# Kernel optimization log

Hardware: AMD Instinct MI355X
Metric: run time of the kernel (lower is better)

The kernel has to match this reference:

```python
import jax, jax.numpy as jnp
import numpy as np

N = 50000
E = 800000
IN_C = 128
HID = 128
OUT_C = 2


def _linear_params(key, fan_in, fan_out):
    k1, k2 = jax.random.split(key)
    bound = 1.0 / np.sqrt(fan_in)
    W = jax.random.uniform(k1, (fan_in, fan_out), jnp.float32, -bound, bound)
    b = jax.random.uniform(k2, (fan_out,), jnp.float32, -bound, bound)
    return W, b


def setup_inputs() -> dict:
    key = jax.random.key(0)
    ks = jax.random.split(key, 9)
    x = jax.random.normal(ks[0], (N, IN_C), jnp.float32)
    edge_index = jax.random.randint(ks[1], (2, E), 0, N, jnp.int64)
    W1a, b1a = _linear_params(ks[2], IN_C, HID)
    W1b, b1b = _linear_params(ks[3], HID, HID)
    W2a, b2a = _linear_params(ks[4], HID, HID)
    W2b, b2b = _linear_params(ks[5], HID, HID)
    Wfc, bfc = _linear_params(ks[6], HID, OUT_C)
    return {
        "x": x, "edge_index": edge_index,
        "W1a": W1a, "b1a": b1a, "W1b": W1b, "b1b": b1b,
        "W2a": W2a, "b2a": b2a, "W2b": W2b, "b2b": b2b,
        "Wfc": Wfc, "bfc": bfc,
    }


def _gin_conv(x, src, dst, Wa, ba, Wb, bb):
    # GINConv with eps=0: h = MLP(x + sum_{j in N(i)} x_j)
    agg = jax.ops.segment_sum(x[src], dst, num_segments=N)  # [N, d]
    h = x + agg
    h = jax.nn.relu(h @ Wa + ba)
    return h @ Wb + bb


def reference(x, edge_index, W1a, b1a, W1b, b1b, W2a, b2a, W2b, b2b, Wfc, bfc):
    src, dst = edge_index[0], edge_index[1]  # messages flow src -> dst
    h = _gin_conv(x, src, dst, W1a, b1a, W1b, b1b)
    h = jax.nn.relu(h)
    # dropout is identity in eval mode
    h = _gin_conv(h, src, dst, W2a, b2a, W2b, b2b)
    return h @ Wfc + bfc  # [N, 2]
```

## Files before the change

### kernel.cpp

```cpp
#include <hip/hip_runtime.h>

#define N_NODES 50000
#define N_EDGES 800000
#define NBUK    196
#define B_A     1024
#define EPB     782
#define CAPB    5120

typedef unsigned short u16;
typedef unsigned int   u32;
typedef __bf16 bf16x8 __attribute__((ext_vector_type(8)));
typedef float  f32x4  __attribute__((ext_vector_type(4)));

__device__ __forceinline__ float bf_lo(u32 v){ return __uint_as_float(v << 16); }
__device__ __forceinline__ float bf_hi(u32 v){ return __uint_as_float(v & 0xffff0000u); }
__device__ __forceinline__ u32 bf_pack(float a, float b){
    u32 ua = __float_as_uint(a), ub = __float_as_uint(b);
    ua += 0x7fffu + ((ua >> 16) & 1u);
    ub += 0x7fffu + ((ub >> 16) & 1u);
    return (ua >> 16) | (ub & 0xffff0000u);
}
__device__ __forceinline__ u16 f2bf(float a){
    u32 ua = __float_as_uint(a);
    ua += 0x7fffu + ((ua >> 16) & 1u);
    return (u16)(ua >> 16);
}
__device__ __forceinline__ void addu4(uint4 v, float* a){
    a[0] += bf_lo(v.x); a[1] += bf_hi(v.x);
    a[2] += bf_lo(v.y); a[3] += bf_hi(v.y);
    a[4] += bf_lo(v.z); a[5] += bf_hi(v.z);
    a[6] += bf_lo(v.w); a[7] += bf_hi(v.w);
}

__device__ __forceinline__ int blockScan256(int v, int* ws, int t) {
    int lane = t & 63, w = t >> 6;
    #pragma unroll
    for (int off = 1; off < 64; off <<= 1) {
        int u = __shfl_up(v, off);
        if (lane >= off) v += u;
    }
    if (lane == 63) ws[w] = v;
    __syncthreads();
    int add = 0;
    for (int k = 0; k < w; k++) add += ws[k];
    return v + add;
}

__launch_bounds__(256)
__global__ void binA_kernel(const int* __restrict__ esrc, const int* __restrict__ edst,
                            u32* __restrict__ binned, int* __restrict__ startTab,
                            int* __restrict__ cntTab,
                            const float* __restrict__ xsrc, u32* __restrict__ xb,
                            const float* __restrict__ W1a, const float* __restrict__ W1b,
                            const float* __restrict__ W2a, const float* __restrict__ W2b,
                            const float* __restrict__ Wfc, const float* __restrict__ b2b,
                            const float* __restrict__ bfc,
                            u16* __restrict__ wt1a, u16* __restrict__ wt1b,
                            u16* __restrict__ wt2a,
                            float* __restrict__ Wc, float* __restrict__ bc) {
    int t = threadIdx.x, blk = blockIdx.x;
    if (blk >= B_A) {
        int b = blk - B_A;
        if (b < 192) {
            int g  = b * 256 + t;
            int mi = g >> 14;
            int p  = g & 16383;
            int k  = p >> 7, m = p & 127;
            const float* src = (mi == 0) ? W1a : (mi == 1) ? W1b : W2a;
            u16* dst         = (mi == 0) ? wt1a : (mi == 1) ? wt1b : wt2a;
            dst[m * 128 + k] = f2bf(src[k * 128 + m]);
        } else {
            int j = t >> 1, o = t & 1;
            float s = 0.f;
            for (int k = 0; k < 128; k++)
                s += W2b[j * 128 + k] * Wfc[k * 2 + o];
            Wc[j * 2 + o] = s;
            if (t < 2) {
                float s2 = 0.f;
                for (int k = 0; k < 128; k++)
                    s2 += b2b[k] * Wfc[k * 2 + t];
                bc[t] = s2 + bfc[t];
            }
        }
        return;
    }
    __shared__ int hist[NBUK];
    __shared__ int cur[NBUK];
    __shared__ u32 ebuf[EPB];
    __shared__ int ws[4];
    int base = blk * EPB;
    for (int i = t; i < NBUK; i += 256) hist[i] = 0;
    __syncthreads();
    for (int i = t; i < EPB; i += 256) {
        int gi = base + i;
        if (gi < N_EDGES) atomicAdd(&hist[edst[gi] >> 8], 1);
    }
    __syncthreads();
    int v = (t < NBUK) ? hist[t] : 0;
    int incl = blockScan256(v, ws, t);
    int excl = incl - v;
    if (t < NBUK) {
        startTab[t * B_A + blk] = excl;
        cntTab[t * B_A + blk]   = v;
        cur[t] = excl;
    }
    __syncthreads();
    for (int i = t; i < EPB; i += 256) {
        int gi = base + i;
        if (gi < N_EDGES) {
            int d = edst[gi], s = esrc[gi];
            int p = atomicAdd(&cur[d >> 8], 1);
            ebuf[p] = (u32)s | ((u32)(d & 255) << 16);
        }
    }
    __syncthreads();
    for (int i = t; i < EPB; i += 256)
        binned[base + i] = ebuf[i];
    const int total = N_NODES * 64;
    for (int i = blk * 256 + t; i < total; i += B_A * 256) {
        float2 f = ((const float2*)xsrc)[i];
        xb[i] = bf_pack(f.x, f.y);
    }
}

__launch_bounds__(256)
__global__ void binB_kernel(const u32* __restrict__ binned, const int* __restrict__ startTab,
                            const int* __restrict__ cntTab,
                            int2* __restrict__ span, int* __restrict__ csr) {
    __shared__ u32 ebuf[CAPB];
    __shared__ int cbuf[CAPB];
    __shared__ int runoff[B_A + 1];
    __shared__ int runstart[B_A];
    __shared__ int hist[256];
    __shared__ int cursor[256];
    __shared__ int ws[4];
    int b = blockIdx.x, t = threadIdx.x;
    int c4[4], s = 0;
    #pragma unroll
    for (int q = 0; q < 4; q++) {
        c4[q] = cntTab[b * B_A + t * 4 + q];
        s += c4[q];
    }
    int incl = blockScan256(s, ws, t);
    int rb = incl - s;
    #pragma unroll
    for (int q = 0; q < 4; q++) {
        int run = t * 4 + q;
        runoff[run]   = rb;
        runstart[run] = run * EPB + startTab[b * B_A + run];
        rb += c4[q];
    }
    if (t == 255) runoff[B_A] = incl;
    hist[t] = 0;
    __syncthreads();
    int tot = runoff[B_A];
    if (tot > CAPB) tot = CAPB;
    for (int i = t; i < tot; i += 256) {
        int lo = 0, hi = B_A;
        while (hi - lo > 1) {
            int mid = (lo + hi) >> 1;
            if (runoff[mid] <= i) lo = mid; else hi = mid;
        }
        ebuf[i] = binned[runstart[lo] + (i - runoff[lo])];
    }
    __syncthreads();
    for (int i = t; i < tot; i += 256)
        atomicAdd(&hist[ebuf[i] >> 16], 1);
    __syncthreads();
    int hv = hist[t];
    int hincl = blockScan256(hv, ws, t);
    int hexcl = hincl - hv;
    cursor[t] = hexcl;
    int gb = b * CAPB;
    int node = (b << 8) + t;
    if (node < N_NODES) span[node] = make_int2(gb + hexcl, gb + hexcl + hv);
    __syncthreads();
    for (int i = t; i < tot; i += 256) {
        u32 e = ebuf[i];
        int p = atomicAdd(&cursor[e >> 16], 1);
        cbuf[p] = (int)(e & 0xFFFFu);
    }
    __syncthreads();
    for (int i = t; i < tot; i += 256)
        csr[gb + i] = cbuf[i];
}

template<int MODE>
__launch_bounds__(256, 4)
__global__ void fconv_kernel(const u32* __restrict__ xb,
                             const u16* __restrict__ WA, const float* __restrict__ bA,
                             const u16* __restrict__ WB, const float* __restrict__ bB,
                             const float* __restrict__ Wc, const float* __restrict__ bc,
                             const int2* __restrict__ span, const int* __restrict__ csr,
                             u16* __restrict__ C, float2* __restrict__ out, int n) {
    __shared__ u16 As[64][136];
    int t = threadIdx.x;
    int row0 = blockIdx.x * 64;
    int w = t >> 6, lane = t & 63;
    int g4 = lane >> 4, l16 = lane & 15;
    const uint4* xp = (const uint4*)xb;
    #pragma unroll
    for (int p = 0; p < 4; p++) {
        int rl = w * 16 + p * 4 + g4;
        int node = row0 + rl;
        float a[8] = {0.f,0.f,0.f,0.f,0.f,0.f,0.f,0.f};
        if (node < n) {
            addu4(xp[(size_t)node * 16 + l16], a);
            int2 sp = span[node];
            int j = sp.x, jend = sp.y;
            for (; j + 8 <= jend; j += 8) {
                int s0 = csr[j],     s1 = csr[j + 1], s2 = csr[j + 2], s3 = csr[j + 3];
                int s4 = csr[j + 4], s5 = csr[j + 5], s6 = csr[j + 6], s7 = csr[j + 7];
                uint4 v0 = xp[(size_t)s0 * 16 + l16], v1 = xp[(size_t)s1 * 16 + l16];
                uint4 v2 = xp[(size_t)s2 * 16 + l16], v3 = xp[(size_t)s3 * 16 + l16];
                uint4 v4 = xp[(size_t)s4 * 16 + l16], v5 = xp[(size_t)s5 * 16 + l16];
                uint4 v6 = xp[(size_t)s6 * 16 + l16], v7 = xp[(size_t)s7 * 16 + l16];
                addu4(v0, a); addu4(v1, a); addu4(v2, a); addu4(v3, a);
                addu4(v4, a); addu4(v5, a); addu4(v6, a); addu4(v7, a);
            }
            for (; j + 4 <= jend; j += 4) {
                int s0 = csr[j], s1 = csr[j + 1], s2 = csr[j + 2], s3 = csr[j + 3];
                uint4 v0 = xp[(size_t)s0 * 16 + l16], v1 = xp[(size_t)s1 * 16 + l16];
                uint4 v2 = xp[(size_t)s2 * 16 + l16], v3 = xp[(size_t)s3 * 16 + l16];
                addu4(v0, a); addu4(v1, a); addu4(v2, a); addu4(v3, a);
            }
            for (; j < jend; j++)
                addu4(xp[(size_t)csr[j] * 16 + l16], a);
        }
        uint4 pk = make_uint4(bf_pack(a[0], a[1]), bf_pack(a[2], a[3]),
                              bf_pack(a[4], a[5]), bf_pack(a[6], a[7]));
        *(uint4*)&As[rl][l16 * 8] = pk;
    }

    int lm = l16, lq = g4;
    f32x4 acc[8];
    #pragma unroll
    for (int c = 0; c < 8; c++) acc[c] = (f32x4){0.f, 0.f, 0.f, 0.f};
    #pragma unroll
    for (int kk = 0; kk < 4; kk++) {
        bf16x8 af = *(const bf16x8*)&As[w * 16 + lm][kk * 32 + lq * 8];
        #pragma unroll
        for (int c = 0; c < 8; c++) {
            bf16x8 bf = *(const bf16x8*)(WA + (size_t)(c * 16 + lm) * 128 + kk * 32 + lq * 8);
            acc[c] = __builtin_amdgcn_mfma_f32_16x16x32_bf16(af, bf, acc[c], 0, 0, 0);
        }
    }
    if (MODE == 0) {
        #pragma unroll
        for (int c = 0; c < 8; c++) {
            int col = c * 16 + lm;
            float bcol = bA[col];
            #pragma unroll
            for (int r = 0; r < 4; r++) {
                float v = acc[c][r] + bcol;
                v = v > 0.f ? v : 0.f;
                As[w * 16 + lq * 4 + r][col] = f2bf(v);
            }
        }
        f32x4 acc2[8];
        #pragma unroll
        for (int c = 0; c < 8; c++) acc2[c] = (f32x4){0.f, 0.f, 0.f, 0.f};
        #pragma unroll
        for (int kk = 0; kk < 4; kk++) {
            bf16x8 af = *(const bf16x8*)&As[w * 16 + lm][kk * 32 + lq * 8];
            #pragma unroll
            for (int c = 0; c < 8; c++) {
                bf16x8 bf = *(const bf16x8*)(WB + (size_t)(c * 16 + lm) * 128 + kk * 32 + lq * 8);
                acc2[c] = __builtin_amdgcn_mfma_f32_16x16x32_bf16(af, bf, acc2[c], 0, 0, 0);
            }
        }
        #pragma unroll
        for (int c = 0; c < 8; c++) {
            int col = c * 16 + lm;
            float bcol = bB[col];
            #pragma unroll
            for (int r = 0; r < 4; r++) {
                int row = row0 + w * 16 + lq * 4 + r;
                if (row < n) {
                    float v = acc2[c][r] + bcol;
                    v = v > 0.f ? v : 0.f;
                    C[(size_t)row * 128 + col] = f2bf(v);
                }
            }
        }
    } else {
        float p0[4] = {0,0,0,0}, p1[4] = {0,0,0,0};
        #pragma unroll
        for (int c = 0; c < 8; c++) {
            int col = c * 16 + lm;
            float bcol = bA[col];
            float2 wc = ((const float2*)Wc)[col];
            #pragma unroll
            for (int r = 0; r < 4; r++) {
                float v = acc[c][r] + bcol;
                v = v > 0.f ? v : 0.f;
                p0[r] += v * wc.x;
                p1[r] += v * wc.y;
            }
        }
        #pragma unroll
        for (int off = 1; off < 16; off <<= 1) {
            #pragma unroll
            for (int r = 0; r < 4; r++) {
                p0[r] += __shfl_xor(p0[r], off);
                p1[r] += __shfl_xor(p1[r], off);
            }
        }
        if (lm == 0) {
            float b0 = bc[0], b1 = bc[1];
            #pragma unroll
            for (int r = 0; r < 4; r++) {
                int row = row0 + w * 16 + lq * 4 + r;
                if (row < n) out[row] = make_float2(p0[r] + b0, p1[r] + b1);
            }
        }
    }
}

extern "C" void kernel_launch(void* const* d_in, const int* in_sizes, int n_in,
                              void* d_out, int out_size, void* d_ws, size_t ws_size,
                              hipStream_t stream) {
    const float* x   = (const float*)d_in[0];
    const int*   ei  = (const int*)d_in[1];
    const float* W1a = (const float*)d_in[2];
    const float* b1a = (const float*)d_in[3];
    const float* W1b = (const float*)d_in[4];
    const float* b1b = (const float*)d_in[5];
    const float* W2a = (const float*)d_in[6];
    const float* b2a = (const float*)d_in[7];
    const float* W2b = (const float*)d_in[8];
    const float* b2b = (const float*)d_in[9];
    const float* Wfc = (const float*)d_in[10];
    const float* bfc = (const float*)d_in[11];

    const int* esrc = ei;
    const int* edst = ei + N_EDGES;

    char* w = (char*)d_ws;
    size_t off = 0;
    auto alloc = [&](size_t bytes) -> char* {
        char* p = w + off;
        off = (off + bytes + 255) & ~(size_t)255;
        return p;
    };
    int2*  span       = (int2*)alloc((size_t)N_NODES * 8);
    int*   startTab   = (int*)alloc((size_t)NBUK * B_A * 4);
    int*   cntTab     = (int*)alloc((size_t)NBUK * B_A * 4);
    int*   csr        = (int*)alloc((size_t)NBUK * CAPB * 4);
    u16*   wt1a       = (u16*)alloc(128 * 128 * 2);
    u16*   wt1b       = (u16*)alloc(128 * 128 * 2);
    u16*   wt2a       = (u16*)alloc(128 * 128 * 2);
    float* Wc         = (float*)alloc(256 * 4);
    float* bc         = (float*)alloc(2 * 4);
    u16*   bufA       = (u16*)alloc((size_t)N_NODES * 128 * 2);
    u16*   bufB       = (u16*)alloc((size_t)N_NODES * 128 * 2);
    u32*   binned     = (u32*)bufA;

    binA_kernel<<<B_A + 193, 256, 0, stream>>>(esrc, edst, binned, startTab, cntTab,
                                               x, (u32*)bufB,
                                               W1a, W1b, W2a, W2b, Wfc, b2b, bfc,
                                               wt1a, wt1b, wt2a, Wc, bc);
    binB_kernel<<<NBUK, 256, 0, stream>>>(binned, startTab, cntTab, span, csr);

    const int TILES = (N_NODES + 63) / 64;
    fconv_kernel<0><<<TILES, 256, 0, stream>>>((const u32*)bufB, wt1a, b1a, wt1b, b1b,
                                               nullptr, nullptr, span, csr,
                                               bufA, nullptr, N_NODES);
    fconv_kernel<1><<<TILES, 256, 0, stream>>>((const u32*)bufA, wt2a, b2a, nullptr, nullptr,
                                               Wc, bc, span, csr,
                                               nullptr, (float2*)d_out, N_NODES);
}
```

Before: 227.9 us.

## Halve bucket width to 128 nodes and gather runs per-thread in binB

The destination buckets shrink from 256 to 128 nodes, doubling the bucket count to 392 so binB launches twice as many smaller blocks with half the shared capacity. binB also drops the per-element binary search over run offsets and has each thread copy its own four runs sequentially. The goal is more parallelism and less shared memory per block in the binning stage. Sequential per-thread copies give uncoalesced, unbalanced loads, and the smaller CAPB raises the risk of bucket overflow truncating edges.

```diff
diff --git a/kernel.cpp b/kernel.cpp
--- a/kernel.cpp
+++ b/kernel.cpp
@@ -2,10 +2,10 @@
 
 #define N_NODES 50000
 #define N_EDGES 800000
-#define NBUK    196
+#define NBUK    392
 #define B_A     1024
 #define EPB     782
-#define CAPB    5120
+#define CAPB    2560
 
 typedef unsigned short u16;
 typedef unsigned int   u32;
@@ -93,24 +93,29 @@
     __syncthreads();
     for (int i = t; i < EPB; i += 256) {
         int gi = base + i;
-        if (gi < N_EDGES) atomicAdd(&hist[edst[gi] >> 8], 1);
-    }
-    __syncthreads();
-    int v = (t < NBUK) ? hist[t] : 0;
-    int incl = blockScan256(v, ws, t);
-    int excl = incl - v;
-    if (t < NBUK) {
-        startTab[t * B_A + blk] = excl;
-        cntTab[t * B_A + blk]   = v;
-        cur[t] = excl;
+        if (gi < N_EDGES) atomicAdd(&hist[edst[gi] >> 7], 1);
+    }
+    __syncthreads();
+    int c0 = 0, c1 = 0;
+    if (t < 196) { c0 = hist[2 * t]; c1 = hist[2 * t + 1]; }
+    int s2 = c0 + c1;
+    int incl = blockScan256(s2, ws, t);
+    int excl = incl - s2;
+    if (t < 196) {
+        startTab[(2 * t) * B_A + blk]     = excl;
+        cntTab[(2 * t) * B_A + blk]       = c0;
+        cur[2 * t] = excl;
+        startTab[(2 * t + 1) * B_A + blk] = excl + c0;
+        cntTab[(2 * t + 1) * B_A + blk]   = c1;
+        cur[2 * t + 1] = excl + c0;
     }
     __syncthreads();
     for (int i = t; i < EPB; i += 256) {
         int gi = base + i;
         if (gi < N_EDGES) {
             int d = edst[gi], s = esrc[gi];
-            int p = atomicAdd(&cur[d >> 8], 1);
-            ebuf[p] = (u32)s | ((u32)(d & 255) << 16);
+            int p = atomicAdd(&cur[d >> 7], 1);
+            ebuf[p] = (u32)s | ((u32)(d & 127) << 16);
         }
     }
     __syncthreads();
@@ -129,51 +134,48 @@
                             int2* __restrict__ span, int* __restrict__ csr) {
     __shared__ u32 ebuf[CAPB];
     __shared__ int cbuf[CAPB];
-    __shared__ int runoff[B_A + 1];
-    __shared__ int runstart[B_A];
-    __shared__ int hist[256];
-    __shared__ int cursor[256];
+    __shared__ int hist[128];
+    __shared__ int cursor[128];
     __shared__ int ws[4];
+    __shared__ int totsh;
     int b = blockIdx.x, t = threadIdx.x;
-    int c4[4], s = 0;
+    int c4[4], rs4[4], s = 0;
     #pragma unroll
     for (int q = 0; q < 4; q++) {
-        c4[q] = cntTab[b * B_A + t * 4 + q];
+        int run = t * 4 + q;
+        c4[q]  = cntTab[b * B_A + run];
+        rs4[q] = run * EPB + startTab[b * B_A + run];
         s += c4[q];
     }
     int incl = blockScan256(s, ws, t);
     int rb = incl - s;
+    if (t == 255) totsh = incl;
+    if (t < 128) hist[t] = 0;
+    __syncthreads();
     #pragma unroll
     for (int q = 0; q < 4; q++) {
-        int run = t * 4 + q;
-        runoff[run]   = rb;
-        runstart[run] = run * EPB + startTab[b * B_A + run];
-        rb += c4[q];
-    }
-    if (t == 255) runoff[B_A] = incl;
-    hist[t] = 0;
-    __syncthreads();
-    int tot = runoff[B_A];
+        int c = c4[q], rs = rs4[q];
+        for (int k = 0; k < c; k++) {
+            int p = rb + k;
+            if (p < CAPB) ebuf[p] = binned[rs + k];
+        }
+        rb += c;
+    }
+    __syncthreads();
+    int tot = totsh;
     if (tot > CAPB) tot = CAPB;
-    for (int i = t; i < tot; i += 256) {
-        int lo = 0, hi = B_A;
-        while (hi - lo > 1) {
-            int mid = (lo + hi) >> 1;
-            if (runoff[mid] <= i) lo = mid; else hi = mid;
-        }
-        ebuf[i] = binned[runstart[lo] + (i - runoff[lo])];
-    }
-    __syncthreads();
     for (int i = t; i < tot; i += 256)
         atomicAdd(&hist[ebuf[i] >> 16], 1);
     __syncthreads();
-    int hv = hist[t];
+    int hv = (t < 128) ? hist[t] : 0;
     int hincl = blockScan256(hv, ws, t);
     int hexcl = hincl - hv;
-    cursor[t] = hexcl;
     int gb = b * CAPB;
-    int node = (b << 8) + t;
-    if (node < N_NODES) span[node] = make_int2(gb + hexcl, gb + hexcl + hv);
+    if (t < 128) {
+        cursor[t] = hexcl;
+        int node = (b << 7) + t;
+        if (node < N_NODES) span[node] = make_int2(gb + hexcl, gb + hexcl + hv);
+    }
     __syncthreads();
     for (int i = t; i < tot; i += 256) {
         u32 e = ebuf[i];
```

Result: no change. 223.7 us (-1.8%).
